# Optimization experiments

Hardware: AMD Instinct MI355X
Metric: run time of the kernel (lower is better)

Reference implementation:

```python
import jax, jax.numpy as jnp
import numpy as np

HEAD_DIM = 128
N_HEADS = 32
NEG_INF = -1e9


def apply_rope(x, cos, sin):
    # x: (B, S, H, D); cos/sin: (S, D//2). Pairs (x[...,2i], x[...,2i+1]) form
    # complex numbers (torch.view_as_complex on reshape(..., -1, 2)).
    xr = x[..., 0::2]
    xi = x[..., 1::2]
    c = cos[None, :, None, :]
    s = sin[None, :, None, :]
    out_r = xr * c - xi * s
    out_i = xr * s + xi * c
    return jnp.stack([out_r, out_i], axis=-1).reshape(x.shape)


def setup_inputs() -> dict:
    key = jax.random.key(0)
    ks = jax.random.split(key, 8)
    B, S, D = 2, 1024, 4096
    hd = HEAD_DIM
    x = jax.random.normal(ks[0], (B, S, D), dtype=jnp.float32)
    # true RoPE frequencies
    theta = 10000.0 ** (-np.arange(0, hd, 2, dtype=np.float32) / hd)  # (hd/2,)
    angles = np.arange(S, dtype=np.float32)[:, None] * theta[None, :]  # (S, hd/2)
    freqs_cos = jnp.asarray(np.cos(angles))
    freqs_sin = jnp.asarray(np.sin(angles))
    # causal additive mask
    mask = jnp.where(jnp.triu(jnp.ones((S, S), dtype=bool), k=1), NEG_INF, 0.0)
    mask = mask[None, None, :, :].astype(jnp.float32)
    scale = 0.02
    wq = jax.random.normal(ks[1], (D, D), dtype=jnp.float32) * scale
    wk = jax.random.normal(ks[2], (D, D), dtype=jnp.float32) * scale
    wv = jax.random.normal(ks[3], (D, D), dtype=jnp.float32) * scale
    wo = jax.random.normal(ks[4], (D, D), dtype=jnp.float32) * scale
    cache_k = jnp.zeros((B, S, N_HEADS, hd), dtype=jnp.float32)
    cache_v = jnp.zeros((B, S, N_HEADS, hd), dtype=jnp.float32)
    return {
        "x": x, "start_pos": 0, "freqs_cos": freqs_cos, "freqs_sin": freqs_sin,
        "mask": mask, "cache_k": cache_k, "cache_v": cache_v,
        "wq": wq, "wk": wk, "wv": wv, "wo": wo,
    }


def reference(x, start_pos, freqs_cos, freqs_sin, mask, cache_k, cache_v, wq, wk, wv, wo):
    B, S, D = x.shape
    H, hd = N_HEADS, HEAD_DIM
    # QKV projections (torch Linear: y = x @ W.T)
    xq = jnp.einsum('bsd,od->bso', x, wq).reshape(B, S, H, hd)
    xk = jnp.einsum('bsd,od->bso', x, wk).reshape(B, S, H, hd)
    xv = jnp.einsum('bsd,od->bso', x, wv).reshape(B, S, H, hd)
    xq = apply_rope(xq, freqs_cos, freqs_sin)
    xk = apply_rope(xk, freqs_cos, freqs_sin)
    # KV-cache append (n_rep == 1, so repeat_kv is identity)
    cache_k = jax.lax.dynamic_update_slice(cache_k, xk, (0, start_pos, 0, 0))
    cache_v = jax.lax.dynamic_update_slice(cache_v, xv, (0, start_pos, 0, 0))
    kv_len = start_pos + S
    keys = cache_k[:, :kv_len]
    values = cache_v[:, :kv_len]
    # attention: energy -> mask -> scaled softmax -> weighted sum
    energy = jnp.einsum('bqhd,bkhd->bhqk', xq, keys)
    energy = energy + mask
    scores = jax.nn.softmax(energy.astype(jnp.float32) / jnp.sqrt(jnp.float32(hd)), axis=-1).astype(xq.dtype)
    out = jnp.einsum('bhqk,bkhd->bqhd', scores, values).reshape(B, S, H * hd)
    return jnp.einsum('bso,do->bsd', out, wo)
```

## Files before the change

### kernel.cpp

```cpp
#include <hip/hip_runtime.h>
#include <hip/hip_bf16.h>
#include <stdint.h>
#include <stddef.h>

typedef __bf16 bf16_t;
typedef __attribute__((ext_vector_type(8))) __bf16 bf16x8;
typedef __attribute__((ext_vector_type(4))) float f32x4;

#define D_MODEL 4096
#define SEQ 1024
#define NH 32
#define HD 128
#define MTOT 2048

#define VMCNT(n) asm volatile("s_waitcnt vmcnt(" #n ")" ::: "memory")
#define SCHED0() __builtin_amdgcn_sched_barrier(0)

__device__ __forceinline__ void gload_lds16(const void* g, void* l) {
  __builtin_amdgcn_global_load_lds((const __attribute__((address_space(1))) uint32_t*)g,
                                   (__attribute__((address_space(3))) uint32_t*)l, 16, 0, 0);
}

__global__ void dtype_probe(const uint32_t* __restrict__ x, uint32_t* __restrict__ flag) {
  const int lane = threadIdx.x & 63;
  const uint32_t w = x[lane];
  const uint32_t e = (w >> 7) & 0xFF;
  const bool inband = (e >= 100 && e <= 140);
  const unsigned long long m = __ballot(inband);
  if (lane == 0) *flag = (__popcll(m) >= 32) ? 1u : 0u;
}

__global__ __launch_bounds__(256) void conv_bf16(const void* __restrict__ src,
                                                 bf16_t* __restrict__ dst, int n,
                                                 const uint32_t* __restrict__ flag) {
  const int i = (blockIdx.x * 256 + threadIdx.x) * 8;
  if (i >= n) return;
  if (*flag) {
    *(bf16x8*)(dst + i) = *(const bf16x8*)((const bf16_t*)src + i);
  } else {
    const float4 a = *(const float4*)((const float*)src + i);
    const float4 b = *(const float4*)((const float*)src + i + 4);
    bf16x8 v;
    v[0] = (bf16_t)a.x; v[1] = (bf16_t)a.y; v[2] = (bf16_t)a.z; v[3] = (bf16_t)a.w;
    v[4] = (bf16_t)b.x; v[5] = (bf16_t)b.y; v[6] = (bf16_t)b.z; v[7] = (bf16_t)b.w;
    *(bf16x8*)(dst + i) = v;
  }
}

template <int MODE>
__global__ __launch_bounds__(512, 2) void gemm_bt(
    const bf16_t* __restrict__ A, const bf16_t* __restrict__ B,
    void* __restrict__ dstv, const uint32_t* __restrict__ flagp) {
  __shared__ __align__(16) char smem[3 * 49152];
  const int tid = threadIdx.x;
  const int lane = tid & 63, wid = tid >> 6;
  const int fr = lane & 15, fq = lane >> 4;
  const int wm = wid >> 2, wn = wid & 3;
  const int bm0 = blockIdx.x * 128, bn0 = blockIdx.y * 256;
  const bool isbf = (MODE == 2) ? (*flagp != 0) : true;

  auto stage = [&](int t, int bi) {
    const int k0 = t * 64;
    char* ab = smem + bi * 49152;
    char* bb = ab + 16384;
#pragma unroll
    for (int j = 0; j < 2; ++j) {
      const int o = j * 8192 + tid * 16;
      const int row = o >> 7, ch = (o >> 4) & 7;
      gload_lds16(A + (size_t)(bm0 + row) * D_MODEL + k0 + ((ch ^ (row & 7)) * 8), ab + o);
    }
#pragma unroll
    for (int j = 0; j < 4; ++j) {
      const int o = j * 8192 + tid * 16;
      const int row = o >> 7, ch = (o >> 4) & 7;
      gload_lds16(B + (size_t)(bn0 + row) * D_MODEL + k0 + ((ch ^ (row & 7)) * 8), bb + o);
    }
  };

  f32x4 acc[4][4];
#pragma unroll
  for (int m = 0; m < 4; m++)
#pragma unroll
    for (int n = 0; n < 4; n++) acc[m][n] = f32x4{0.f, 0.f, 0.f, 0.f};

  auto compute = [&](int bi) {
    const char* ab = smem + bi * 49152;
    const char* bb = ab + 16384;
#pragma unroll
    for (int kk = 0; kk < 2; ++kk) {
      const int swz = ((kk * 4 + fq) ^ (fr & 7)) << 4;
      bf16x8 af[4], bfv[4];
#pragma unroll
      for (int m = 0; m < 4; ++m)
        af[m] = *(const bf16x8*)(ab + (wm * 64 + m * 16 + fr) * 128 + swz);
#pragma unroll
      for (int n = 0; n < 4; ++n)
        bfv[n] = *(const bf16x8*)(bb + (wn * 64 + n * 16 + fr) * 128 + swz);
      __builtin_amdgcn_s_setprio(1);
#pragma unroll
      for (int m = 0; m < 4; ++m)
#pragma unroll
        for (int n = 0; n < 4; ++n)
          acc[m][n] = __builtin_amdgcn_mfma_f32_16x16x32_bf16(af[m], bfv[n], acc[m][n], 0, 0, 0);
      __builtin_amdgcn_s_setprio(0);
    }
  };

  const int NT = D_MODEL / 64;
  stage(0, 0);
  stage(1, 1);
  int cur = 0, nxt = 2;
  for (int t = 0; t < NT - 2; ++t) {
    stage(t + 2, nxt);
    VMCNT(12);
    __builtin_amdgcn_s_barrier();
    SCHED0();
    compute(cur);
    __builtin_amdgcn_s_barrier();
    SCHED0();
    cur = (cur == 2) ? 0 : cur + 1;
    nxt = (nxt == 2) ? 0 : nxt + 1;
  }
  VMCNT(6);
  __builtin_amdgcn_s_barrier();
  SCHED0();
  compute(cur);
  __builtin_amdgcn_s_barrier();
  SCHED0();
  cur = (cur == 2) ? 0 : cur + 1;
  VMCNT(0);
  __builtin_amdgcn_s_barrier();
  SCHED0();
  compute(cur);

#pragma unroll
  for (int m = 0; m < 4; m++) {
#pragma unroll
    for (int n = 0; n < 4; n++) {
      const int gn = bn0 + wn * 64 + n * 16 + fr;
#pragma unroll
      for (int r = 0; r < 4; r++) {
        const int gm = bm0 + wm * 64 + m * 16 + fq * 4 + r;
        const float vv = acc[m][n][r];
        if constexpr (MODE == 0) {
          const int b = gm >> 10, s = gm & (SEQ - 1), h = gn >> 7, dd = gn & (HD - 1);
          ((bf16_t*)dstv)[((size_t)(b * NH + h) * SEQ + s) * HD + dd] = (bf16_t)vv;
        } else if constexpr (MODE == 1) {
          const int b = gm >> 10, s = gm & (SEQ - 1), h = gn >> 7, dd = gn & (HD - 1);
          ((bf16_t*)dstv)[((size_t)(b * NH + h) * HD + dd) * SEQ + s] = (bf16_t)vv;
        } else {
          if (isbf) ((bf16_t*)dstv)[(size_t)gm * D_MODEL + gn] = (bf16_t)vv;
          else      ((float*)dstv)[(size_t)gm * D_MODEL + gn] = vv;
        }
      }
    }
  }
}

__global__ __launch_bounds__(256) void rope_kernel(
    bf16_t* __restrict__ q, bf16_t* __restrict__ k,
    const bf16_t* __restrict__ fcos, const bf16_t* __restrict__ fsin) {
  const int PT = MTOT * (D_MODEL / 2);
  const int p = blockIdx.x * blockDim.x + threadIdx.x;
  bf16_t* buf = (p < PT) ? q : k;
  const int pp = p & (PT - 1);
  const int s = (pp >> 6) & (SEQ - 1);
  const int i = pp & 63;
  const float c = (float)fcos[s * 64 + i];
  const float si = (float)fsin[s * 64 + i];
  const float x0 = (float)buf[2 * (size_t)pp];
  const float x1 = (float)buf[2 * (size_t)pp + 1];
  buf[2 * (size_t)pp] = (bf16_t)(x0 * c - x1 * si);
  buf[2 * (size_t)pp + 1] = (bf16_t)(x0 * si + x1 * c);
}

__global__ __launch_bounds__(256, 3) void attn_fwd(
    const bf16_t* __restrict__ Q, const bf16_t* __restrict__ K,
    const bf16_t* __restrict__ V, bf16_t* __restrict__ Out) {
  constexpr float SC = 0.088388347648318447f;
  constexpr float MNEG = -10000.0f;
  __shared__ __align__(16) bf16_t Kt[64][136];
  __shared__ __align__(16) bf16_t Vt[128][72];
  __shared__ __align__(16) bf16_t Pb[4][16][72];
  const int tid = threadIdx.x, lane = tid & 63, wid = tid >> 6;
  const int fr = lane & 15, fq = lane >> 4;
  const int qt = (int)gridDim.x - 1 - blockIdx.x;
  const int bh = blockIdx.y;
  const int q0 = qt * 64 + wid * 16;

  const bf16_t* Kbase = K + (size_t)bh * SEQ * HD;
  const bf16_t* Vbase = V + (size_t)bh * HD * SEQ;

  bf16x8 qa[4];
  {
    const bf16_t* qp = Q + ((size_t)bh * SEQ + q0 + fr) * HD + fq * 8;
#pragma unroll
    for (int ks = 0; ks < 4; ++ks) qa[ks] = *(const bf16x8*)(qp + ks * 32);
  }
  f32x4 Oacc[8];
#pragma unroll
  for (int i = 0; i < 8; i++) Oacc[i] = f32x4{0.f, 0.f, 0.f, 0.f};
  float mrow[4] = {MNEG, MNEG, MNEG, MNEG};
  float lrow[4] = {0.f, 0.f, 0.f, 0.f};

  bf16x8 kreg[4], vreg[4];
  auto issue = [&](int kv0) {
#pragma unroll
    for (int j = 0; j < 4; ++j) {
      const int idx = j * 256 + tid;
      kreg[j] = *(const bf16x8*)(Kbase + (size_t)(kv0 + (idx >> 4)) * HD + (idx & 15) * 8);
      vreg[j] = *(const bf16x8*)(Vbase + (size_t)(idx >> 3) * SEQ + kv0 + (idx & 7) * 8);
    }
  };
  auto commit = [&]() {
#pragma unroll
    for (int j = 0; j < 4; ++j) {
      const int idx = j * 256 + tid;
      *(bf16x8*)&Kt[idx >> 4][(idx & 15) * 8] = kreg[j];
      *(bf16x8*)&Vt[idx >> 3][(idx & 7) * 8] = vreg[j];
    }
  };

  const int nt = qt + 1;
  issue(0);
  commit();
  __syncthreads();

  for (int t = 0; t < nt; ++t) {
    const bool last = (t == nt - 1);
    if (!last) issue((t + 1) * 64);

    f32x4 sacc[4];
#pragma unroll
    for (int nb = 0; nb < 4; ++nb) sacc[nb] = f32x4{0.f, 0.f, 0.f, 0.f};
    __builtin_amdgcn_s_setprio(1);
#pragma unroll
    for (int nb = 0; nb < 4; ++nb) {
      const int kvc = nb * 16 + fr;
#pragma unroll
      for (int ks = 0; ks < 4; ++ks) {
        bf16x8 kb = *(const bf16x8*)&Kt[kvc][(ks * 4 + fq) * 8];
        sacc[nb] = __builtin_amdgcn_mfma_f32_16x16x32_bf16(qa[ks], kb, sacc[nb], 0, 0, 0);
      }
    }
    __builtin_amdgcn_s_setprio(0);

    float xv[4][4], al[4];
#pragma unroll
    for (int r = 0; r < 4; ++r) {
      const int qrow = q0 + fq * 4 + r;
#pragma unroll
      for (int nb = 0; nb < 4; ++nb) {
        const float xx = sacc[nb][r] * SC;
        xv[nb][r] = (!last || (t * 64 + nb * 16 + fr) <= qrow) ? xx : MNEG;
      }
      float pm = fmaxf(fmaxf(xv[0][r], xv[1][r]), fmaxf(xv[2][r], xv[3][r]));
      pm = fmaxf(pm, __shfl_xor(pm, 1));
      pm = fmaxf(pm, __shfl_xor(pm, 2));
      pm = fmaxf(pm, __shfl_xor(pm, 4));
      pm = fmaxf(pm, __shfl_xor(pm, 8));
      const float mn = fmaxf(mrow[r], pm);
      al[r] = __expf(mrow[r] - mn);
      mrow[r] = mn;
      float ps = 0.f;
#pragma unroll
      for (int nb = 0; nb < 4; ++nb) {
        const float pv = __expf(xv[nb][r] - mn);
        xv[nb][r] = pv;
        ps += pv;
      }
      lrow[r] = lrow[r] * al[r] + ps;
    }
#pragma unroll
    for (int db = 0; db < 8; ++db)
#pragma unroll
      for (int r = 0; r < 4; ++r) Oacc[db][r] *= al[r];

#pragma unroll
    for (int nb = 0; nb < 4; ++nb)
#pragma unroll
      for (int r = 0; r < 4; ++r)
        Pb[wid][fq * 4 + r][nb * 16 + fr] = (bf16_t)xv[nb][r];
    bf16x8 pa0 = *(const bf16x8*)&Pb[wid][fr][fq * 8];
    bf16x8 pa1 = *(const bf16x8*)&Pb[wid][fr][32 + fq * 8];

    __builtin_amdgcn_s_setprio(1);
#pragma unroll
    for (int db = 0; db < 8; ++db) {
      const int d = db * 16 + fr;
      bf16x8 vb0 = *(const bf16x8*)&Vt[d][fq * 8];
      bf16x8 vb1 = *(const bf16x8*)&Vt[d][32 + fq * 8];
      Oacc[db] = __builtin_amdgcn_mfma_f32_16x16x32_bf16(pa0, vb0, Oacc[db], 0, 0, 0);
      Oacc[db] = __builtin_amdgcn_mfma_f32_16x16x32_bf16(pa1, vb1, Oacc[db], 0, 0, 0);
    }
    __builtin_amdgcn_s_setprio(0);

    if (!last) {
      __syncthreads();
      commit();
      __syncthreads();
    }
  }

  float linv[4];
#pragma unroll
  for (int r = 0; r < 4; ++r) {
    float ps = lrow[r];
    ps += __shfl_xor(ps, 1);
    ps += __shfl_xor(ps, 2);
    ps += __shfl_xor(ps, 4);
    ps += __shfl_xor(ps, 8);
    linv[r] = 1.0f / fmaxf(ps, 1e-20f);
  }

  const int b = bh >> 5, h = bh & 31;
#pragma unroll
  for (int db = 0; db < 8; ++db) {
    const int d = db * 16 + fr;
#pragma unroll
    for (int r = 0; r < 4; ++r) {
      const int q = q0 + fq * 4 + r;
      Out[((size_t)(b * SEQ + q)) * D_MODEL + h * HD + d] = (bf16_t)(Oacc[db][r] * linv[r]);
    }
  }
}

extern "C" void kernel_launch(void* const* d_in, const int* in_sizes, int n_in,
                              void* d_out, int out_size, void* d_ws, size_t ws_size,
                              hipStream_t stream) {
  (void)in_sizes; (void)n_in; (void)out_size;
  const void* x_raw    = d_in[0];
  const void* fcos_raw = d_in[2];
  const void* fsin_raw = d_in[3];
  const void* wq_raw   = d_in[7];
  const void* wk_raw   = d_in[8];
  const void* wv_raw   = d_in[9];
  const void* wo_raw   = d_in[10];

  const size_t NX = (size_t)MTOT * D_MODEL;
  const size_t NW = (size_t)D_MODEL * D_MODEL;
  const size_t NF = SEQ * (HD / 2);

  char* base = (char*)d_ws;
  uint32_t* flag = (uint32_t*)base;
  bf16_t* fc = (bf16_t*)(base + 4096);
  bf16_t* fs = (bf16_t*)(base + 4096 + 131072);
  bf16_t* elems = (bf16_t*)(base + (1 << 20));
  bf16_t* xc = elems;
  bf16_t* w0 = xc + NX;
  bf16_t* w1 = w0 + NW;
  bf16_t* q_ws = w1 + NW;
  bf16_t* k_ws = q_ws + NX;
  bf16_t* v_ws = k_ws + NX;
  bf16_t* a_ws = v_ws + NX;
  const size_t NEED = (1 << 20) + 2 * (5 * NX + 2 * NW);
  if (ws_size < NEED) return;

  dtype_probe<<<1, 64, 0, stream>>>((const uint32_t*)x_raw, flag);

  const int cb_x = (int)(NX / (256 * 8));
  const int cb_w = (int)(NW / (256 * 8));
  const int cb_f = (int)(NF / (256 * 8));
  conv_bf16<<<cb_x, 256, 0, stream>>>(x_raw, xc, (int)NX, flag);
  conv_bf16<<<cb_f, 256, 0, stream>>>(fcos_raw, fc, (int)NF, flag);
  conv_bf16<<<cb_f, 256, 0, stream>>>(fsin_raw, fs, (int)NF, flag);

  dim3 gg(MTOT / 128, D_MODEL / 256);
  conv_bf16<<<cb_w, 256, 0, stream>>>(wq_raw, w0, (int)NW, flag);
  gemm_bt<0><<<gg, 512, 0, stream>>>(xc, w0, q_ws, flag);
  conv_bf16<<<cb_w, 256, 0, stream>>>(wk_raw, w1, (int)NW, flag);
  gemm_bt<0><<<gg, 512, 0, stream>>>(xc, w1, k_ws, flag);
  conv_bf16<<<cb_w, 256, 0, stream>>>(wv_raw, w0, (int)NW, flag);
  gemm_bt<1><<<gg, 512, 0, stream>>>(xc, w0, v_ws, flag);

  rope_kernel<<<(2 * MTOT * (D_MODEL / 2)) / 256, 256, 0, stream>>>(q_ws, k_ws, fc, fs);
  attn_fwd<<<dim3(SEQ / 64, 2 * NH), 256, 0, stream>>>(q_ws, k_ws, v_ws, a_ws);

  conv_bf16<<<cb_w, 256, 0, stream>>>(wo_raw, w1, (int)NW, flag);
  gemm_bt<2><<<gg, 512, 0, stream>>>(a_ws, w1, d_out, flag);
}
```

Baseline: 456.7 us.

## Split GEMM k-tile into two phases interleaving half-stage loads with MFMA

Restructures the bf16 GEMM main loop so each 64-wide k-tile is processed in two phases. Each phase issues its LDS fragment reads, then half of the next tile's global-to-LDS loads, then a barrier and an lgkmcnt wait before the MFMA block. The goal is to spread global-load issue across the compute and overlap LDS reads with prefetch, instead of issuing all loads in one burst before compute. It adds extra barriers per tile, which may cost synchronization overhead.

```diff
diff --git a/kernel.cpp b/kernel.cpp
--- a/kernel.cpp
+++ b/kernel.cpp
@@ -14,6 +14,7 @@
 #define MTOT 2048
 
 #define VMCNT(n) asm volatile("s_waitcnt vmcnt(" #n ")" ::: "memory")
+#define LGKM0() asm volatile("s_waitcnt lgkmcnt(0)" ::: "memory")
 #define SCHED0() __builtin_amdgcn_sched_barrier(0)
 
 __device__ __forceinline__ void gload_lds16(const void* g, void* l) {
@@ -59,19 +60,18 @@
   const int bm0 = blockIdx.x * 128, bn0 = blockIdx.y * 256;
   const bool isbf = (MODE == 2) ? (*flagp != 0) : true;
 
-  auto stage = [&](int t, int bi) {
+  auto stage_half = [&](int t, int bi, int h) {
     const int k0 = t * 64;
     char* ab = smem + bi * 49152;
     char* bb = ab + 16384;
-#pragma unroll
-    for (int j = 0; j < 2; ++j) {
-      const int o = j * 8192 + tid * 16;
+    {
+      const int o = h * 8192 + tid * 16;
       const int row = o >> 7, ch = (o >> 4) & 7;
       gload_lds16(A + (size_t)(bm0 + row) * D_MODEL + k0 + ((ch ^ (row & 7)) * 8), ab + o);
     }
 #pragma unroll
-    for (int j = 0; j < 4; ++j) {
-      const int o = j * 8192 + tid * 16;
+    for (int j = 0; j < 2; ++j) {
+      const int o = (h * 2 + j) * 8192 + tid * 16;
       const int row = o >> 7, ch = (o >> 4) & 7;
       gload_lds16(B + (size_t)(bn0 + row) * D_MODEL + k0 + ((ch ^ (row & 7)) * 8), bb + o);
     }
@@ -83,55 +83,57 @@
 #pragma unroll
     for (int n = 0; n < 4; n++) acc[m][n] = f32x4{0.f, 0.f, 0.f, 0.f};
 
-  auto compute = [&](int bi) {
+  auto phase = [&](int bi, int kk, bool do_stage, int ts, int bs, int h) {
     const char* ab = smem + bi * 49152;
     const char* bb = ab + 16384;
-#pragma unroll
-    for (int kk = 0; kk < 2; ++kk) {
-      const int swz = ((kk * 4 + fq) ^ (fr & 7)) << 4;
-      bf16x8 af[4], bfv[4];
-#pragma unroll
-      for (int m = 0; m < 4; ++m)
-        af[m] = *(const bf16x8*)(ab + (wm * 64 + m * 16 + fr) * 128 + swz);
+    const int swz = ((kk * 4 + fq) ^ (fr & 7)) << 4;
+    bf16x8 af[4], bfv[4];
+#pragma unroll
+    for (int m = 0; m < 4; ++m)
+      af[m] = *(const bf16x8*)(ab + (wm * 64 + m * 16 + fr) * 128 + swz);
+#pragma unroll
+    for (int n = 0; n < 4; ++n)
+      bfv[n] = *(const bf16x8*)(bb + (wn * 64 + n * 16 + fr) * 128 + swz);
+    if (do_stage) stage_half(ts, bs, h);
+    __builtin_amdgcn_s_barrier();
+    LGKM0();
+    SCHED0();
+    __builtin_amdgcn_s_setprio(1);
+#pragma unroll
+    for (int m = 0; m < 4; ++m)
 #pragma unroll
       for (int n = 0; n < 4; ++n)
-        bfv[n] = *(const bf16x8*)(bb + (wn * 64 + n * 16 + fr) * 128 + swz);
-      __builtin_amdgcn_s_setprio(1);
-#pragma unroll
-      for (int m = 0; m < 4; ++m)
-#pragma unroll
-        for (int n = 0; n < 4; ++n)
-          acc[m][n] = __builtin_amdgcn_mfma_f32_16x16x32_bf16(af[m], bfv[n], acc[m][n], 0, 0, 0);
-      __builtin_amdgcn_s_setprio(0);
-    }
+        acc[m][n] = __builtin_amdgcn_mfma_f32_16x16x32_bf16(af[m], bfv[n], acc[m][n], 0, 0, 0);
+    __builtin_amdgcn_s_setprio(0);
   };
 
   const int NT = D_MODEL / 64;
-  stage(0, 0);
-  stage(1, 1);
+  stage_half(0, 0, 0); stage_half(0, 0, 1);
+  stage_half(1, 1, 0); stage_half(1, 1, 1);
+  VMCNT(6);
+  __builtin_amdgcn_s_barrier();
+  SCHED0();
   int cur = 0, nxt = 2;
   for (int t = 0; t < NT - 2; ++t) {
-    stage(t + 2, nxt);
-    VMCNT(12);
+    phase(cur, 0, true, t + 2, nxt, 0);
     __builtin_amdgcn_s_barrier();
-    SCHED0();
-    compute(cur);
+    phase(cur, 1, true, t + 2, nxt, 1);
+    VMCNT(6);
     __builtin_amdgcn_s_barrier();
     SCHED0();
     cur = (cur == 2) ? 0 : cur + 1;
     nxt = (nxt == 2) ? 0 : nxt + 1;
   }
-  VMCNT(6);
+  phase(cur, 0, false, 0, 0, 0);
   __builtin_amdgcn_s_barrier();
-  SCHED0();
-  compute(cur);
+  phase(cur, 1, false, 0, 0, 0);
+  VMCNT(0);
   __builtin_amdgcn_s_barrier();
   SCHED0();
   cur = (cur == 2) ? 0 : cur + 1;
-  VMCNT(0);
+  phase(cur, 0, false, 0, 0, 0);
   __builtin_amdgcn_s_barrier();
-  SCHED0();
-  compute(cur);
+  phase(cur, 1, false, 0, 0, 0);
 
 #pragma unroll
   for (int m = 0; m < 4; m++) {
```

Result: faster. 438.9 us (-3.9%).
